# Performance work log

Hardware: AMD Instinct MI355X
Metric: run time of the kernel (lower is better)

The kernel has to match this reference:

```python
import jax, jax.numpy as jnp
import numpy as np

B, S, D, H = 4, 1024, 1024, 16
DH = D // H
LN_EPS = 1e-5


def setup_inputs() -> dict:
    key = jax.random.key(0)
    ks = jax.random.split(key, 12)
    lim = 1.0 / np.sqrt(D)
    u = lambda k, shp: jax.random.uniform(k, shp, jnp.float32, -lim, lim)
    return {
        "x": jax.random.normal(ks[0], (B, S, D), jnp.float32),
        "Wq": u(ks[1], (D, D)), "bq": u(ks[2], (D,)),
        "Wk": u(ks[3], (D, D)), "bk": u(ks[4], (D,)),
        "Wv": u(ks[5], (D, D)), "bv": u(ks[6], (D,)),
        "Wo": u(ks[7], (D, D)), "bo": u(ks[8], (D,)),
        "gamma": jnp.ones((D,), jnp.float32),
        "beta": jnp.zeros((D,), jnp.float32),
    }


def _layer_norm(x, gamma, beta):
    mu = jnp.mean(x, axis=-1, keepdims=True)
    var = jnp.mean(jnp.square(x - mu), axis=-1, keepdims=True)
    return (x - mu) * jax.lax.rsqrt(var + LN_EPS) * gamma + beta


def reference(x, Wq, bq, Wk, bk, Wv, bv, Wo, bo, gamma, beta):
    # Linear projections (torch Linear: x @ W^T + b)
    Q = x @ Wq.T + bq  # [B, S, D]
    K = x @ Wk.T + bk
    V = x @ Wv.T + bv
    # Faithful to original: raw view(B*H, S, DH) with NO head transpose
    Q = Q.reshape(B * H, S, DH)
    K = K.reshape(B * H, S, DH)
    V = V.reshape(B * H, S, DH)
    scale = DH ** -0.5
    attn = jnp.einsum('bqd,bkd->bqk', Q, K) * scale  # [B*H, S, S]
    attn = jax.nn.softmax(attn, axis=-1)
    ctx = jnp.einsum('bqk,bkd->bqd', attn, V)  # [B*H, S, DH]
    ctx = ctx.reshape(B, S, D)
    out = ctx @ Wo.T + bo
    out = out + x  # residual (dropout p=0.0 is identity)
    return _layer_norm(out, gamma, beta)
```

## Files before the change

### kernel.cpp

```cpp
#include <hip/hip_runtime.h>
#include <hip/hip_bf16.h>


using u16 = unsigned short;
using u32 = unsigned int;
typedef __attribute__((ext_vector_type(8)))  short bf16x8;
typedef __attribute__((ext_vector_type(4)))  float f32x4;
typedef __attribute__((ext_vector_type(16))) float f32x16;
typedef __attribute__((ext_vector_type(4)))  u16  u16x4;
typedef __attribute__((ext_vector_type(8)))  u16  u16x8;

#define AS1C(p) ((const __attribute__((address_space(1))) void*)(p))
#define AS3(p)  ((__attribute__((address_space(3))) void*)(p))

__device__ __forceinline__ u16 f2bf(float f) {
  union { float f; unsigned u; } v; v.f = f;
  unsigned u = v.u;
  return (u16)((u + 0x7fffu + ((u >> 16) & 1u)) >> 16);
}

__device__ __forceinline__ u32 pk_bf16(float a, float b) {
  u32 r;
  asm("v_cvt_pk_bf16_f32 %0, %1, %2" : "=v"(r) : "v"(a), "v"(b));
  return r;
}
__device__ __forceinline__ float exp2fast(float x) {
  float r;
  asm("v_exp_f32 %0, %1" : "=v"(r) : "v"(x));
  return r;
}
__device__ __forceinline__ float bf2f(u16 b) {
  union { u32 u; float f; } v; v.u = ((u32)b) << 16; return v.f;
}

__device__ __forceinline__ f32x4 mfma16(bf16x8 a, bf16x8 b, f32x4 c) {
  return __builtin_amdgcn_mfma_f32_16x16x32_bf16(a, b, c, 0, 0, 0);
}
__device__ __forceinline__ f32x16 mfma32(bf16x8 a, bf16x8 b, f32x16 c) {
  return __builtin_amdgcn_mfma_f32_32x32x16_bf16(a, b, c, 0, 0, 0);
}

__global__ __launch_bounds__(256) void prep_kernel(
    const float* __restrict__ x,
    const float* __restrict__ wq, const float* __restrict__ wk,
    const float* __restrict__ wv, const float* __restrict__ wo,
    const float* __restrict__ bq, const float* __restrict__ bk, const float* __restrict__ bv,
    u16* __restrict__ xb, u16* __restrict__ wb, float* __restrict__ bc)
{
  int ch = blockIdx.x * 256 + threadIdx.x;
  if (ch < 2097152) {
    const float* src; u16* dst;
    if (ch < 1048576) { src = x + ch * 4; dst = xb + ch * 4; }
    else {
      int c2 = ch - 1048576;
      int wsel = c2 >> 18;
      int off  = c2 & 262143;
      const float* wsrc[4] = { wq, wk, wv, wo };
      src = wsrc[wsel] + off * 4;
      dst = wb + wsel * 1048576 + off * 4;
    }
    f32x4 v = *(const f32x4*)src;
    union { u32 u[2]; u16x4 v4; } o;
    o.u[0] = pk_bf16(v[0], v[1]);
    o.u[1] = pk_bf16(v[2], v[3]);
    *(u16x4*)dst = o.v4;
  } else {
    int c3 = ch - 2097152;
    int bsel = c3 >> 8, off = c3 & 255;
    const float* bsrc[3] = { bq, bk, bv };
    f32x4 v = *(const f32x4*)(bsrc[bsel] + off * 4);
    *(f32x4*)(bc + bsel * 1024 + off * 4) = v;
  }
}

__global__ __launch_bounds__(256) void gemm_qkv(
    const u16* __restrict__ A, const u16* __restrict__ Bw,
    const float* __restrict__ bias, u16* __restrict__ outb)
{
  __shared__ u16 As[3][4096];
  __shared__ u16 Bs[3][4096];

  const int K = 1024;
  int tid = threadIdx.x, w = tid >> 6, lane = tid & 63;
  int g = lane >> 4, lr = lane & 15;
  int wr = w >> 1, wcn = w & 1;

  int bid = blockIdx.x;
  int bm = (bid & 7) + 8 * ((bid >> 3) & 3);
  int bn = bid >> 5;

  int ch0 = tid, ch1 = tid + 256;
  auto srcoff = [&](int ch) -> size_t {
    int r = ch >> 2, pc = ch & 3;
    int gc = pc ^ ((r >> 2) & 3);
    return (size_t)r * K + gc * 8;
  };
  const u16* aS0 = A  + (size_t)(bm * 128) * K + srcoff(ch0);
  const u16* aS1 = A  + (size_t)(bm * 128) * K + srcoff(ch1);
  const u16* bS0 = Bw + (size_t)(bn * 128) * K + srcoff(ch0);
  const u16* bS1 = Bw + (size_t)(bn * 128) * K + srcoff(ch1);
  int lo0 = ch0 * 8, lo1 = ch1 * 8;

  auto STAGE = [&](int buf, int kt) {
    __builtin_amdgcn_global_load_lds(AS1C(aS0 + kt * 32), AS3(&As[buf][lo0]), 16, 0, 0);
    __builtin_amdgcn_global_load_lds(AS1C(aS1 + kt * 32), AS3(&As[buf][lo1]), 16, 0, 0);
    __builtin_amdgcn_global_load_lds(AS1C(bS0 + kt * 32), AS3(&Bs[buf][lo0]), 16, 0, 0);
    __builtin_amdgcn_global_load_lds(AS1C(bS1 + kt * 32), AS3(&Bs[buf][lo1]), 16, 0, 0);
  };

  f32x4 acc[4][4] = {};
  int pc8 = (g ^ ((lr >> 2) & 3)) * 8;

  auto COMPUTE = [&](int buf) {
    bf16x8 af[4], bfr[4];
#pragma unroll
    for (int m = 0; m < 4; ++m)
      af[m] = *(const bf16x8*)&As[buf][(wr * 64 + m * 16 + lr) * 32 + pc8];
#pragma unroll
    for (int n = 0; n < 4; ++n)
      bfr[n] = *(const bf16x8*)&Bs[buf][(wcn * 64 + n * 16 + lr) * 32 + pc8];
    __builtin_amdgcn_s_setprio(1);
#pragma unroll
    for (int m = 0; m < 4; ++m)
#pragma unroll
      for (int n = 0; n < 4; ++n)
        acc[m][n] = mfma16(af[m], bfr[n], acc[m][n]);
    __builtin_amdgcn_s_setprio(0);
  };

  STAGE(0, 0); STAGE(1, 1);

  int sb = 2, cb = 0;
  for (int t = 0; t < 31; ++t) {
    asm volatile("s_waitcnt vmcnt(4)" ::: "memory");
    __builtin_amdgcn_s_barrier();
    asm volatile("" ::: "memory");
    if (t < 30) {
      STAGE(sb, t + 2);
      if (++sb == 3) sb = 0;
    }
    COMPUTE(cb);
    if (++cb == 3) cb = 0;
  }
  asm volatile("s_waitcnt vmcnt(0)" ::: "memory");
  __builtin_amdgcn_s_barrier();
  asm volatile("" ::: "memory");
  COMPUTE(cb);

#pragma unroll
  for (int m = 0; m < 4; ++m) {
    int row0 = bm * 128 + wr * 64 + m * 16 + 4 * g;
#pragma unroll
    for (int n = 0; n < 4; ++n) {
      int col = bn * 128 + wcn * 64 + n * 16 + lr;
#pragma unroll
      for (int i = 0; i < 4; ++i) {
        float v = acc[m][n][i] + bias[col];
        int r = row0 + i;
        if (col < 1024) {
          outb[(size_t)r * 1024 + col] = f2bf(v * 0.18033688f);
        } else if (col < 2048) {
          outb[4194304 + (size_t)r * 1024 + (col - 1024)] = f2bf(v);
        } else {
          int c = col - 2048;
          outb[8388608 + (size_t)(r >> 6) * 65536 + (size_t)(c & 63) * 1024
               + (r & 63) * 16 + (c >> 6)] = f2bf(v);
        }
      }
    }
  }
}

__global__ __launch_bounds__(256) void gemm_op(
    const u16* __restrict__ A, const u16* __restrict__ Bw,
    const float* __restrict__ bias, u16* __restrict__ outp)
{
  __shared__ u16 As[3][2048];
  __shared__ u16 Bs[3][4096];

  const int K = 1024;
  int tid = threadIdx.x, w = tid >> 6, lane = tid & 63;
  int g = lane >> 4, lr = lane & 15;
  int wr = w >> 1, wcn = w & 1;
  int bid = blockIdx.x;
  int bm = bid & 63, bn = bid >> 6;

  auto srcoff = [&](int ch) -> size_t {
    int r = ch >> 2, pc = ch & 3;
    int gc = pc ^ ((r >> 2) & 3);
    return (size_t)r * K + gc * 8;
  };
  const u16* aS0 = A  + (size_t)(bm * 64)  * K + srcoff(tid);
  const u16* bS0 = Bw + (size_t)(bn * 128) * K + srcoff(tid);
  const u16* bS1 = Bw + (size_t)(bn * 128) * K + srcoff(tid + 256);

  auto STAGE = [&](int buf, int kt) {
    __builtin_amdgcn_global_load_lds(AS1C(aS0 + kt * 32), AS3(&As[buf][tid * 8]),        16, 0, 0);
    __builtin_amdgcn_global_load_lds(AS1C(bS0 + kt * 32), AS3(&Bs[buf][tid * 8]),        16, 0, 0);
    __builtin_amdgcn_global_load_lds(AS1C(bS1 + kt * 32), AS3(&Bs[buf][2048 + tid * 8]), 16, 0, 0);
  };

  f32x4 acc[2][4] = {};
  int pc8 = (g ^ ((lr >> 2) & 3)) * 8;

  auto COMPUTE = [&](int buf) {
    bf16x8 af[2], bfr[4];
#pragma unroll
    for (int m = 0; m < 2; ++m)
      af[m] = *(const bf16x8*)&As[buf][(wr * 32 + m * 16 + lr) * 32 + pc8];
#pragma unroll
    for (int n = 0; n < 4; ++n)
      bfr[n] = *(const bf16x8*)&Bs[buf][(wcn * 64 + n * 16 + lr) * 32 + pc8];
    __builtin_amdgcn_s_setprio(1);
#pragma unroll
    for (int m = 0; m < 2; ++m)
#pragma unroll
      for (int n = 0; n < 4; ++n)
        acc[m][n] = mfma16(af[m], bfr[n], acc[m][n]);
    __builtin_amdgcn_s_setprio(0);
  };

  STAGE(0, 0); STAGE(1, 1);

  int sb = 2, cb = 0;
  for (int t = 0; t < 31; ++t) {
    asm volatile("s_waitcnt vmcnt(3)" ::: "memory");
    __builtin_amdgcn_s_barrier();
    asm volatile("" ::: "memory");
    if (t < 30) {
      STAGE(sb, t + 2);
      if (++sb == 3) sb = 0;
    }
    COMPUTE(cb);
    if (++cb == 3) cb = 0;
  }
  asm volatile("s_waitcnt vmcnt(0)" ::: "memory");
  __builtin_amdgcn_s_barrier();
  asm volatile("" ::: "memory");
  COMPUTE(cb);

#pragma unroll
  for (int m = 0; m < 2; ++m) {
    int row0 = bm * 64 + wr * 32 + m * 16 + 4 * g;
#pragma unroll
    for (int n = 0; n < 4; ++n) {
      int col = bn * 128 + wcn * 64 + n * 16 + lr;
#pragma unroll
      for (int i = 0; i < 4; ++i)
        outp[(size_t)(row0 + i) * 1024 + col] = f2bf(acc[m][n][i] + bias[col]);
    }
  }
}

__global__ __launch_bounds__(256) void attn_kernel(
    const u16* __restrict__ Qb, const u16* __restrict__ Kb,
    const u16* __restrict__ Vtb, u16* __restrict__ Ob)
{
  __shared__ u16 Ks[3][4096];
  __shared__ u16 Vts[3][4096];

  int blk = blockIdx.x;
  int bh = blk & 63, qt = blk >> 6;
  int tid = threadIdx.x, wid = tid >> 6, lane = tid & 63;
  int l31 = lane & 31, hi = lane >> 5;

  const u16* Qp = Qb  + (size_t)bh * 65536;
  const u16* Kp = Kb  + (size_t)bh * 65536;
  const u16* Vp = Vtb + (size_t)bh * 65536;

  int q = qt * 128 + wid * 32 + l31;

  bf16x8 qf[4];
#pragma unroll
  for (int s = 0; s < 4; ++s)
    qf[s] = *(const bf16x8*)&Qp[(size_t)q * 64 + s * 16 + hi * 8];

  f32x16 oacc[2] = {};
  float mrow = -3e38f, lrow = 0.f;

  const u16* gk[2]; const u16* gv[2];
#pragma unroll
  for (int j = 0; j < 2; ++j) {
    int ch = tid + 256 * j;
    int kc = ch >> 3, scc = ch & 7;
    int sc = scc ^ (kc & 7);
    gk[j] = Kp + (size_t)kc * 64   + sc * 8;
    gv[j] = Vp + (size_t)kc * 1024 + sc * 8;
  }

  auto STAGE = [&](int buf, int kt) {
#pragma unroll
    for (int j = 0; j < 2; ++j) {
      int ch = tid + 256 * j;
      __builtin_amdgcn_global_load_lds(AS1C(gk[j] + (size_t)kt * 4096), AS3(&Ks[buf][ch * 8]),  16, 0, 0);
      __builtin_amdgcn_global_load_lds(AS1C(gv[j] + kt * 64),           AS3(&Vts[buf][ch * 8]), 16, 0, 0);
    }
  };

  STAGE(0, 0); STAGE(1, 1);

  int sb = 2, cb = 0;
  for (int kt = 0; kt < 16; ++kt) {
    if (kt < 15) { asm volatile("s_waitcnt vmcnt(4)" ::: "memory"); }
    else         { asm volatile("s_waitcnt vmcnt(0)" ::: "memory"); }
    __builtin_amdgcn_s_barrier();
    asm volatile("" ::: "memory");
    if (kt < 14) {
      STAGE(sb, kt + 2);
      if (++sb == 3) sb = 0;
    }

    f32x16 s2[2];
#pragma unroll
    for (int ks = 0; ks < 2; ++ks) {
      f32x16 z = {};
      int row = ks * 32 + l31;
      int rx = (row & 7);
      __builtin_amdgcn_s_setprio(1);
#pragma unroll
      for (int s = 0; s < 4; ++s) {
        bf16x8 kb = *(const bf16x8*)&Ks[cb][row * 64 + (((2 * s + hi) ^ rx) * 8)];
        z = mfma32(kb, qf[s], z);
      }
      __builtin_amdgcn_s_setprio(0);
      s2[ks] = z;
    }

    float tv[16];
#pragma unroll
    for (int r = 0; r < 16; ++r) tv[r] = fmaxf(s2[0][r], s2[1][r]);
#pragma unroll
    for (int st = 8; st > 0; st >>= 1)
#pragma unroll
      for (int r = 0; r < st; ++r) tv[r] = fmaxf(tv[r], tv[r + st]);
    float tm = fmaxf(tv[0], __shfl_xor(tv[0], 32));

    bool nores = __all(tm - mrow <= 11.0f);
    float mn, corr;
    if (nores) { mn = mrow; corr = 1.f; }
    else       { mn = fmaxf(mrow, tm); corr = exp2fast(mrow - mn); }

    float sv[16];
#pragma unroll
    for (int r = 0; r < 16; ++r) {
      s2[0][r] = exp2fast(s2[0][r] - mn);
      s2[1][r] = exp2fast(s2[1][r] - mn);
      sv[r] = s2[0][r] + s2[1][r];
    }
#pragma unroll
    for (int st = 8; st > 0; st >>= 1)
#pragma unroll
      for (int r = 0; r < st; ++r) sv[r] += sv[r + st];
    float rs = sv[0] + __shfl_xor(sv[0], 32);

    if (nores) {
      lrow += rs;
    } else {
#pragma unroll
      for (int dt = 0; dt < 2; ++dt)
#pragma unroll
        for (int r = 0; r < 16; ++r) oacc[dt][r] *= corr;
      lrow = lrow * corr + rs;
      mrow = mn;
    }

    u32 wpk[2][4][2];
#pragma unroll
    for (int ks = 0; ks < 2; ++ks)
#pragma unroll
      for (int r1 = 0; r1 < 4; ++r1)
#pragma unroll
        for (int p = 0; p < 2; ++p)
          wpk[ks][r1][p] = pk_bf16(s2[ks][4 * r1 + 2 * p], s2[ks][4 * r1 + 2 * p + 1]);

#pragma unroll
    for (int s = 0; s < 4; ++s) {
      int ks = s >> 1, t = s & 1;
      u32 a0 = wpk[ks][2 * t][0],     a1 = wpk[ks][2 * t][1];
      u32 b0 = wpk[ks][2 * t + 1][0], b1 = wpk[ks][2 * t + 1][1];
      u32 sa0 = (u32)__shfl_xor((int)a0, 32), sa1 = (u32)__shfl_xor((int)a1, 32);
      u32 sb0 = (u32)__shfl_xor((int)b0, 32), sb1 = (u32)__shfl_xor((int)b1, 32);
      union { u32 u[4]; bf16x8 v; } pb;
      pb.u[0] = hi ? sb0 : a0;
      pb.u[1] = hi ? sb1 : a1;
      pb.u[2] = hi ? b0 : sa0;
      pb.u[3] = hi ? b1 : sa1;
      __builtin_amdgcn_s_setprio(1);
#pragma unroll
      for (int dt = 0; dt < 2; ++dt) {
        int row = dt * 32 + l31;
        bf16x8 vb = *(const bf16x8*)&Vts[cb][row * 64 + (((2 * s + hi) ^ (row & 7)) * 8)];
        oacc[dt] = mfma32(vb, pb.v, oacc[dt]);
      }
      __builtin_amdgcn_s_setprio(0);
    }

    if (++cb == 3) cb = 0;
  }

  float inv = 1.f / lrow;
  u16* Op = Ob + (size_t)bh * 65536 + (size_t)q * 64;
#pragma unroll
  for (int dt = 0; dt < 2; ++dt)
#pragma unroll
    for (int rq = 0; rq < 4; ++rq) {
      int d0 = dt * 32 + 8 * rq + 4 * hi;
      union { u32 u[2]; u16x4 v; } o4;
      o4.u[0] = pk_bf16(oacc[dt][4 * rq + 0] * inv, oacc[dt][4 * rq + 1] * inv);
      o4.u[1] = pk_bf16(oacc[dt][4 * rq + 2] * inv, oacc[dt][4 * rq + 3] * inv);
      *(u16x4*)&Op[d0] = o4.v;
    }
}

__global__ __launch_bounds__(256) void ln_kernel(
    const float* __restrict__ xres, const u16* __restrict__ proj,
    float* __restrict__ out,
    const float* __restrict__ gamma, const float* __restrict__ beta)
{
  int row = blockIdx.x, tid = threadIdx.x;
  int lane = tid & 63, wid = tid >> 6;
  f32x4 xv = *(const f32x4*)&xres[(size_t)row * 1024 + tid * 4];
  u16x4 pv = *(const u16x4*)&proj[(size_t)row * 1024 + tid * 4];
  f32x4 v;
#pragma unroll
  for (int j = 0; j < 4; ++j) v[j] = xv[j] + bf2f(pv[j]);
  float s = v[0] + v[1] + v[2] + v[3];
  float q = v[0] * v[0] + v[1] * v[1] + v[2] * v[2] + v[3] * v[3];
#pragma unroll
  for (int ms = 1; ms < 64; ms <<= 1) { s += __shfl_xor(s, ms); q += __shfl_xor(q, ms); }
  __shared__ float red[8];
  if (lane == 0) { red[wid] = s; red[wid + 4] = q; }
  __syncthreads();
  s = red[0] + red[1] + red[2] + red[3];
  q = red[4] + red[5] + red[6] + red[7];
  float mu = s * (1.f / 1024.f);
  float var = q * (1.f / 1024.f) - mu * mu;
  float inv = rsqrtf(var + 1e-5f);
  f32x4 g4 = *(const f32x4*)&gamma[tid * 4];
  f32x4 b4 = *(const f32x4*)&beta[tid * 4];
  f32x4 o;
#pragma unroll
  for (int j = 0; j < 4; ++j) o[j] = (v[j] - mu) * inv * g4[j] + b4[j];
  *(f32x4*)&out[(size_t)row * 1024 + tid * 4] = o;
}

extern "C" void kernel_launch(void* const* d_in, const int* in_sizes, int n_in,
                              void* d_out, int out_size, void* d_ws, size_t ws_size,
                              hipStream_t stream) {
  const float* x     = (const float*)d_in[0];
  const float* Wq    = (const float*)d_in[1];
  const float* bq    = (const float*)d_in[2];
  const float* Wk    = (const float*)d_in[3];
  const float* bk    = (const float*)d_in[4];
  const float* Wv    = (const float*)d_in[5];
  const float* bv    = (const float*)d_in[6];
  const float* Wo    = (const float*)d_in[7];
  const float* bo    = (const float*)d_in[8];
  const float* gamma = (const float*)d_in[9];
  const float* beta  = (const float*)d_in[10];
  float* out = (float*)d_out;

  char* ws = (char*)d_ws;
  u16*   xb  = (u16*)ws;
  u16*   wb  = (u16*)(ws + (8u << 20));
  float* bc  = (float*)(ws + (16u << 20));
  u16*   qkv = (u16*)(ws + (16u << 20) + 16384);
  u16*   ctx = xb;
  u16*   proj = qkv;

  prep_kernel<<<8195, 256, 0, stream>>>(x, Wq, Wk, Wv, Wo, bq, bk, bv, xb, wb, bc);

  gemm_qkv<<<768, 256, 0, stream>>>(xb, wb, bc, qkv);

  attn_kernel<<<512, 256, 0, stream>>>(qkv, qkv + 4194304, qkv + 8388608, ctx);

  gemm_op<<<512, 256, 0, stream>>>(ctx, wb + 3 * 1048576, bo, proj);

  ln_kernel<<<4096, 256, 0, stream>>>(x, proj, out, gamma, beta);
}
```

Baseline: 122.6 us.

## Load K/V fragments directly from global into registers, dropping LDS staging

The attention kernel no longer stages K and V tiles through a triple-buffered LDS ring with barriers. Each wave now reads its K and V MFMA fragments straight from global memory into registers, and K for the next tile is prefetched into a ping-pong register buffer. This removes LDS traffic and block-wide barriers. In exchange, the four waves of a block each load the same K/V data redundantly from global memory or L2, and register pressure rises.

```diff
diff --git a/kernel.cpp b/kernel.cpp
--- a/kernel.cpp
+++ b/kernel.cpp
@@ -256,9 +256,6 @@
     const u16* __restrict__ Qb, const u16* __restrict__ Kb,
     const u16* __restrict__ Vtb, u16* __restrict__ Ob)
 {
-  __shared__ u16 Ks[3][4096];
-  __shared__ u16 Vts[3][4096];
-
   int blk = blockIdx.x;
   int bh = blk & 63, qt = blk >> 6;
   int tid = threadIdx.x, wid = tid >> 6, lane = tid & 63;
@@ -278,53 +275,37 @@
   f32x16 oacc[2] = {};
   float mrow = -3e38f, lrow = 0.f;
 
-  const u16* gk[2]; const u16* gv[2];
-#pragma unroll
-  for (int j = 0; j < 2; ++j) {
-    int ch = tid + 256 * j;
-    int kc = ch >> 3, scc = ch & 7;
-    int sc = scc ^ (kc & 7);
-    gk[j] = Kp + (size_t)kc * 64   + sc * 8;
-    gv[j] = Vp + (size_t)kc * 1024 + sc * 8;
-  }
-
-  auto STAGE = [&](int buf, int kt) {
-#pragma unroll
-    for (int j = 0; j < 2; ++j) {
-      int ch = tid + 256 * j;
-      __builtin_amdgcn_global_load_lds(AS1C(gk[j] + (size_t)kt * 4096), AS3(&Ks[buf][ch * 8]),  16, 0, 0);
-      __builtin_amdgcn_global_load_lds(AS1C(gv[j] + kt * 64),           AS3(&Vts[buf][ch * 8]), 16, 0, 0);
-    }
-  };
-
-  STAGE(0, 0); STAGE(1, 1);
-
-  int sb = 2, cb = 0;
-  for (int kt = 0; kt < 16; ++kt) {
-    if (kt < 15) { asm volatile("s_waitcnt vmcnt(4)" ::: "memory"); }
-    else         { asm volatile("s_waitcnt vmcnt(0)" ::: "memory"); }
-    __builtin_amdgcn_s_barrier();
-    asm volatile("" ::: "memory");
-    if (kt < 14) {
-      STAGE(sb, kt + 2);
-      if (++sb == 3) sb = 0;
-    }
-
+  const u16* kbase = Kp + (size_t)l31 * 64 + hi * 8;
+  const u16* vbase = Vp + (size_t)l31 * 1024 + hi * 8;
+
+  auto LOADK = [&](bf16x8 (&kf)[2][4], int kt) {
+#pragma unroll
+    for (int ks = 0; ks < 2; ++ks)
+#pragma unroll
+      for (int s = 0; s < 4; ++s)
+        kf[ks][s] = *(const bf16x8*)&kbase[kt * 4096 + ks * 2048 + s * 16];
+  };
+
+  auto BODY = [&](bf16x8 (&cur)[2][4], bf16x8 (&nxt)[2][4], int kt) {
     f32x16 s2[2];
 #pragma unroll
     for (int ks = 0; ks < 2; ++ks) {
       f32x16 z = {};
-      int row = ks * 32 + l31;
-      int rx = (row & 7);
       __builtin_amdgcn_s_setprio(1);
 #pragma unroll
-      for (int s = 0; s < 4; ++s) {
-        bf16x8 kb = *(const bf16x8*)&Ks[cb][row * 64 + (((2 * s + hi) ^ rx) * 8)];
-        z = mfma32(kb, qf[s], z);
-      }
+      for (int s = 0; s < 4; ++s)
+        z = mfma32(cur[ks][s], qf[s], z);
       __builtin_amdgcn_s_setprio(0);
       s2[ks] = z;
     }
+
+    if (kt + 1 < 16) LOADK(nxt, kt + 1);
+    bf16x8 vf[2][4];
+#pragma unroll
+    for (int dt = 0; dt < 2; ++dt)
+#pragma unroll
+      for (int s = 0; s < 4; ++s)
+        vf[dt][s] = *(const bf16x8*)&vbase[(size_t)dt * 32768 + kt * 64 + s * 16];
 
     float tv[16];
 #pragma unroll
@@ -387,15 +368,17 @@
       pb.u[3] = hi ? b1 : sa1;
       __builtin_amdgcn_s_setprio(1);
 #pragma unroll
-      for (int dt = 0; dt < 2; ++dt) {
-        int row = dt * 32 + l31;
-        bf16x8 vb = *(const bf16x8*)&Vts[cb][row * 64 + (((2 * s + hi) ^ (row & 7)) * 8)];
-        oacc[dt] = mfma32(vb, pb.v, oacc[dt]);
-      }
+      for (int dt = 0; dt < 2; ++dt)
+        oacc[dt] = mfma32(vf[dt][s], pb.v, oacc[dt]);
       __builtin_amdgcn_s_setprio(0);
     }
-
-    if (++cb == 3) cb = 0;
+  };
+
+  bf16x8 kfA[2][4], kfB[2][4];
+  LOADK(kfA, 0);
+  for (int t2 = 0; t2 < 8; ++t2) {
+    BODY(kfA, kfB, 2 * t2);
+    BODY(kfB, kfA, 2 * t2 + 1);
   }
 
   float inv = 1.f / lrow;
```

Result: slower. 150.4 us (median of 5 runs) (+22.7%).
